# Performance work log

Measured on AMD Instinct MI355X. Metric: run time of the kernel, lower is better.

Reference implementation:

```python
import jax, jax.numpy as jnp
import numpy as np

B, T, N, F = 8, 24, 207, 16
H = 64            # hidden_dim
DH = 16           # dims_hyper[-1] / node-embedding out
DA = 4 * F        # temporal attention dim_out
DS = 64           # ss_gal gcn out dim (last_ss_gal_dim)
GDEP = 2
ALPHA, BETA, GAMMA = 0.05, 0.95, 0.95
TA = 2.0


def _lin(x, w, b=None):
    y = x @ w
    return y if b is None else y + b


def gcn_hyper(x, A, W, b):
    # x: [B,N,C], A: [N,N] static. h <- a*x + g * einsum('nvc,vw->nwc', h, A)
    h = x
    outs = [h]
    for _ in range(GDEP):
        h = ALPHA * x + GAMMA * jnp.einsum('bvc,vw->bwc', h, A)
        outs.append(h)
    return _lin(jnp.concatenate(outs, axis=-1), W, b)


def gcn_gru(x, A_dyn, A_sta, W, b):
    # x: [B,N,C], A_dyn: [B,N,N], A_sta: [N,N]
    h = x
    outs = [h]
    for _ in range(GDEP):
        h = (ALPHA * x
             + BETA * jnp.einsum('bvw,bvc->bwc', A_dyn, h)     # bmm(A^T, h)
             + GAMMA * jnp.einsum('bvc,vw->bwc', h, A_sta))
        outs.append(h)
    return _lin(jnp.concatenate(outs, axis=-1), W, b)


def gcn_ssgal(x, A, W, b):
    # x: [B*,N,C], A: [B*,N,N]
    h = x
    outs = [h]
    for _ in range(GDEP):
        h = ALPHA * x + GAMMA * jnp.einsum('bvw,bvc->bwc', A, h)
        outs.append(h)
    return _lin(jnp.concatenate(outs, axis=-1), W, b)


def setup_inputs() -> dict:
    key = jax.random.key(0)
    ks = jax.random.split(key, 32)
    i = iter(range(32))
    w = lambda *s: (0.02 * jax.random.normal(ks[next(i)], s, dtype=jnp.float32))
    inp = {
        'input_sequence': jax.random.normal(ks[next(i)], (B, T, N, F), dtype=jnp.float32),
        'static_adj': jax.random.uniform(ks[next(i)], (N, N), dtype=jnp.float32),
        # hyper graph generators: mlp in = (GDEP+1)*H -> DH
        'src_gen_w': w((GDEP + 1) * H, DH), 'src_gen_b': w(DH),
        'tgt_gen_w': w((GDEP + 1) * H, DH), 'tgt_gen_b': w(DH),
        # node embeddings: F -> DH
        'src_emb_w': w(F, DH), 'src_emb_b': w(DH),
        'tgt_emb_w': w(F, DH), 'tgt_emb_b': w(DH),
        # GRU gate GCNs: mlp in = (GDEP+1)*(F+H) -> H
        'gru_z_w': w((GDEP + 1) * (F + H), H), 'gru_z_b': w(H),
        'gru_r_w': w((GDEP + 1) * (F + H), H), 'gru_r_b': w(H),
        'gru_c_w': w((GDEP + 1) * (F + H), H), 'gru_c_b': w(H),
        # temporal attention: F -> DA, score DA -> 1
        'attn_q_w': w(F, DA),
        'attn_k_w': w(F, DA), 'attn_k_b': w(DA),
        'attn_s_w': w(DA, 1),
        # ss_gal spatial gcn: (GDEP+1)*F -> DS
        'sgcn_w': w((GDEP + 1) * F, DS), 'sgcn_b': w(DS),
        # predictors
        'short_w': w(DS, F), 'short_b': w(F),
        'long_w': w(H, F), 'long_b': w(F),
        'fus_w': w(DS + H, F), 'fus_b': w(F),
    }
    return inp


def _forward(input_sequence, static_adj,
             src_gen_w, src_gen_b, tgt_gen_w, tgt_gen_b,
             src_emb_w, src_emb_b, tgt_emb_w, tgt_emb_b,
             gru_z_w, gru_z_b, gru_r_w, gru_r_b, gru_c_w, gru_c_b,
             attn_q_w, attn_k_w, attn_k_b, attn_s_w,
             sgcn_w, sgcn_b,
             short_w, short_b, long_w, long_b, fus_w, fus_b):
    batch, steps, nodes = input_sequence.shape[0], input_sequence.shape[1], input_sequence.shape[2]
    eye = jnp.eye(nodes, dtype=input_sequence.dtype)

    def cell(x_t, h):
        # x_t: [B,N,F], h: [B,N,H]
        src_ctx = gcn_hyper(h, static_adj, src_gen_w, src_gen_b)   # [B,N,DH]
        tgt_ctx = gcn_hyper(h, static_adj, tgt_gen_w, tgt_gen_b)
        s = jnp.tanh(TA * _lin(x_t, src_emb_w, src_emb_b) * src_ctx)
        t = jnp.tanh(TA * _lin(x_t, tgt_emb_w, tgt_emb_b) * tgt_ctx)
        asym = jnp.einsum('bnc,bmc->bnm', s, t) - jnp.einsum('bnc,bmc->bnm', t, s)
        adj = jax.nn.relu(jnp.tanh(TA * asym)) + eye
        adj = adj / (adj.sum(axis=-1, keepdims=True) + 1e-8)
        gi = jnp.concatenate([x_t, h], axis=-1)
        z = jax.nn.sigmoid(gcn_gru(gi, adj, static_adj, gru_z_w, gru_z_b))
        r = jax.nn.sigmoid(gcn_gru(gi, adj, static_adj, gru_r_w, gru_r_b))
        ri = jnp.concatenate([x_t, r * h], axis=-1)
        c = jnp.tanh(gcn_gru(ri, adj, static_adj, gru_c_w, gru_c_b))
        return z * h + (1.0 - z) * c

    h = jnp.zeros((batch, nodes, H), dtype=input_sequence.dtype)
    for t_step in range(0, max(1, steps - 4), 4):
        h = cell(input_sequence[:, t_step], h)

    # ss_gal branch on the last 4 steps
    recent = input_sequence[:, -4:]            # [B,4,N,F]
    target = input_sequence[:, -1]             # [B,N,F]
    # temporal attention
    q = target @ attn_q_w                      # [B,N,DA]
    k = recent @ attn_k_w + attn_k_b           # [B,4,N,DA]
    scores = jnp.tanh(q[:, None, :, None, :] + k[:, :, None, :, :])  # [B,4,N,N,DA]
    scores = jnp.squeeze(scores @ attn_s_w, axis=-1)                  # [B,4,N,N]
    attn = jax.nn.softmax(scores, axis=-1)
    dyn_adj = static_adj[None] + attn.reshape(-1, nodes, nodes)       # [B*4,N,N]
    rh = recent.reshape(-1, nodes, recent.shape[-1])                  # [B*4,N,F]
    rh = gcn_ssgal(rh, dyn_adj, sgcn_w, sgcn_b)                       # [B*4,N,DS]
    rh = jax.nn.relu(rh.reshape(batch, -1, nodes, rh.shape[-1]))      # [B,4,N,DS]
    target = jnp.sum(rh, axis=1)                                       # [B,N,DS]

    short = _lin(target, short_w, short_b)      # [B,N,F]
    h = cell(short, h)                          # final GRU step on short-term prediction
    long = _lin(h, long_w, long_b)              # [B,N,F]
    fused = _lin(jnp.concatenate([target, h], axis=-1), fus_w, fus_b)  # [B,N,F]
    return jnp.stack([short, long, fused], axis=0)  # [3,B,N,F]


def reference(input_sequence, static_adj,
              src_gen_w, src_gen_b, tgt_gen_w, tgt_gen_b,
              src_emb_w, src_emb_b, tgt_emb_w, tgt_emb_b,
              gru_z_w, gru_z_b, gru_r_w, gru_r_b, gru_c_w, gru_c_b,
              attn_q_w, attn_k_w, attn_k_b, attn_s_w,
              sgcn_w, sgcn_b,
              short_w, short_b, long_w, long_b, fus_w, fus_b):
    return _forward(input_sequence, static_adj,
                    src_gen_w, src_gen_b, tgt_gen_w, tgt_gen_b,
                    src_emb_w, src_emb_b, tgt_emb_w, tgt_emb_b,
                    gru_z_w, gru_z_b, gru_r_w, gru_r_b, gru_c_w, gru_c_b,
                    attn_q_w, attn_k_w, attn_k_b, attn_s_w,
                    sgcn_w, sgcn_b,
                    short_w, short_b, long_w, long_b, fus_w, fus_b)
```

## Files before the change

### kernel.cpp

```cpp
#include <hip/hip_runtime.h>


constexpr int B = 8, T = 24, N = 207, F = 16, H = 64, DH = 16;
constexpr int PS = 208;
constexpr float ALPHA = 0.05f, BETA = 0.95f, GAMMA = 0.95f, TA = 2.0f;
constexpr int NF = N * F;
constexpr int BNF = B * N * F;

__device__ __forceinline__ float tanh_fast(float x) { float e = __expf(2.f * x); return 1.f - 2.f / (e + 1.f); }
__device__ __forceinline__ float sigm(float x) { return 1.f / (1.f + __expf(-x)); }
__device__ __forceinline__ float tanh_poly(float x) {
    float x2 = x * x;
    float c = __builtin_fmaf(x2, 0.13333333f, -0.33333333f);
    return x * __builtin_fmaf(x2, c, 1.f);
}

__global__ __launch_bounds__(256) void k_stage0(
    const float* __restrict__ adj, const float* __restrict__ inp,
    const float* __restrict__ Wq, const float* __restrict__ Wk,
    const float* __restrict__ kb, const float* __restrict__ sw_,
    float* __restrict__ Ts, float* __restrict__ A2,
    float* __restrict__ attnT, float* __restrict__ rsum)
{
    __shared__ __align__(16) float smem[7424];
// ... 163 lines not shown
        for (int k = 0; k < 2; k++) {
            float4 hv = make_float4(0, 0, 0, 0);
            int v = v0 + hr[k];
            if (v < N) hv = *(const float4*)&hb[(size_t)v * H + hc[k]];
            h4[k] = hv;
        }
    };
    loadT(0);
    int cur = 0;
    for (int t = 0; t < 7; t++) {
        __syncthreads();
        {
            float (*dst)[33] = (tid < 128) ? sTs[cur] : sA2[cur];
            dst[pr][pc4] = t4.x; dst[pr][pc4 + 1] = t4.y; dst[pr][pc4 + 2] = t4.z; dst[pr][pc4 + 3] = t4.w;
        }
#pragma unroll
        for (int k = 0; k < 2; k++) *(float4*)&sH[cur][hr[k]][hc[k]] = h4[k];
        if (t < 6) loadT((t + 1) * 32);
        __syncthreads();
#pragma unroll 8
        for (int v = 0; v < 32; v++) {
            float pu = sTs[cur][ty][v], pw = sA2[cur][ty][v];
#pragma unroll
            for (int j = 0; j < 4; j++) {
                float x = sH[cur][v][tx * 4 + j];
                au[j] += pu * x; aw[j] += pw * x;
            }
        }
        cur ^= 1;
    }
    int w = w0 + ty;
    bool valid = w < N;
    __syncthreads();
    if (valid) {
#pragma unroll
        for (int j = 0; j < 4; j++) {
            int c = tx * 4 + j;
            float hv = hb[(size_t)w * H + c];
            float u = au[j], w2 = aw[j];
            cat[ty][c] = hv;
            cat[ty][64 + c] = ALPHA * hv + GAMMA * u;
            cat[ty][128 + c] = ALPHA * hv + ALPHA * GAMMA * u + GAMMA * GAMMA * w2;
        }
    } else {
#pragma unroll
        for (int j = 0; j < 4; j++) {
            int c = tx * 4 + j;
            cat[ty][c] = 0; cat[ty][64 + c] = 0; cat[ty][128 + c] = 0;
        }
    }
    const float* Wg = lane ? Wtgt : Wsrc;
    const float* bg = lane ? btgt : bsrc;
    const float* We = lane ? Wet : Wes;
    const float* be = lane ? bet : bes;
    {
        float4 wv[3];
#pragma unroll
        for (int k = 0; k < 3; k++) wv[k] = *(const float4*)&Wg[(tid + k * 256) * 4];
        float4 xv = make_float4(0, 0, 0, 0), ev = make_float4(0, 0, 0, 0);
        int sr = 0, sc = 0;
        if (tid < 64) {
            sr = tid >> 2; sc = (tid & 3) * 4;
            int n = w0 + sr;
            if (n < N) xv = *(const float4*)&xp[(size_t)n * F + sc];
            ev = *(const float4*)&We[tid * 4];
        }
#pragma unroll
        for (int k = 0; k < 3; k++) {
            int l4 = tid + k * 256;
            int r = l4 >> 2, c4 = (l4 & 3) * 4;
            *(float4*)&sW[r][c4] = wv[k];
        }
        if (tid < 64) {
            *(float4*)&sX[sr][sc] = xv;
            *(float4*)&sWe[sr][sc] = ev;
        }
    }
    __syncthreads();
    if (lane == 0 && valid) {
#pragma unroll
        for (int j = 0; j < 5; j++) {
            int c = tx * 5 + j;
            float v = (c < 16) ? sX[ty][c] : hb[(size_t)w * H + (c - 16)];
            catg[((size_t)(b * N + w)) * 240 + c] = v;
        }
    }
    {
        float ctx = bg[tx];
#pragma unroll 8
        for (int c = 0; c < 192; c++) ctx += cat[ty][c] * sW[c][tx];
        float xe = be[tx];
#pragma unroll
        for (int f = 0; f < 16; f++) xe += sX[ty][f] * sWe[f][tx];
        if (valid) {
            float val = tanh_fast(TA * xe * ctx);
            if (lane == 0) s_out[(size_t)(b * N + w) * DH + tx] = val;
            else           t_out[(size_t)(b * N + w) * DH + tx] = val;
        }
    }
}

__global__ __launch_bounds__(256) void k_cell_bP(const float* __restrict__ s_in, const float* __restrict__ t_in,
                                                 const float* __restrict__ adj, float* __restrict__ P) {
    int b = blockIdx.y, v0 = blockIdx.x * 16;
    int tid = threadIdx.x, ty = tid >> 4, tx = tid & 15;
    __shared__ float sS[N][17], sT[N][17];
    for (int l4 = tid; l4 < 828; l4 += 256) {
        float4 sv = *(const float4*)&s_in[(size_t)b * N * 16 + l4 * 4];
        float4 tv = *(const float4*)&t_in[(size_t)b * N * 16 + l4 * 4];
        int r = l4 >> 2, c = (l4 & 3) * 4;
        sS[r][c] = sv.x; sS[r][c + 1] = sv.y; sS[r][c + 2] = sv.z; sS[r][c + 3] = sv.w;
        sT[r][c] = tv.x; sT[r][c + 1] = tv.y; sT[r][c + 2] = tv.z; sT[r][c + 3] = tv.w;
    }
    __syncthreads();
    int v = v0 + ty;
    bool valid = v < N;
    int vc = valid ? v : (N - 1);
    float sv[16], tv[16];
#pragma unroll
    for (int k = 0; k < 16; k++) { sv[k] = sS[vc][k]; tv[k] = sT[vc][k]; }
    float val[13];
    float rsum = 0.f;
#pragma unroll
    for (int idx = 0; idx < 13; idx++) {
        int w = tx + 16 * idx;
        float r = 0.f;
        if (w < N) {
            float a = 0.f;
#pragma unroll
            for (int k = 0; k < 16; k++) a += sv[k] * sT[w][k] - tv[k] * sS[w][k];
            r = tanh_fast(TA * a);
            r = r > 0.f ? r : 0.f;
            if (w == v) r += 1.f;
        }
        val[idx] = r;
        rsum += r;
    }
    float tot = rsum;
    for (int d = 8; d > 0; d >>= 1) tot += __shfl_down(tot, d, 16);
    tot = __shfl(tot, 0, 16);
    float rinv = BETA / (tot + 1e-8f);
    if (valid) {
        float* Pb = P + (size_t)b * PS * PS;
#pragma unroll
        for (int idx = 0; idx < 13; idx++) {
            int w = tx + 16 * idx;
            if (w < N) Pb[(size_t)w * PS + v] = val[idx] * rinv + GAMMA * adj[v * N + w];
        }
    }
}

__global__ __launch_bounds__(256) void k_prop1(const float* __restrict__ P, float* __restrict__ cat) {
    int b = blockIdx.y, w0 = blockIdx.x * 16, c0 = blockIdx.z * 16;
    int tid = threadIdx.x, ty = tid >> 4, tx = tid & 15;
    const float* Pb = P + (size_t)b * PS * PS;
    __shared__ float sP[2][16][33], sX[2][32][17];
    float a1 = 0.f;
    int pr = tid >> 4, pc = (tid & 15) * 2;
    int xr = tid >> 3, xc = (tid & 7) * 2;
    float2 pv, xv;
    auto loadT = [&](int v0) {
        pv = make_float2(0, 0); xv = make_float2(0, 0);
        int w = w0 + pr;
        if (w < N) pv = *(const float2*)&Pb[(size_t)w * PS + v0 + pc];
        int vv = v0 + xr;
        if (vv < N) xv = *(const float2*)&cat[((size_t)(b * N + vv)) * 240 + c0 + xc];
    };
    loadT(0);
    int cur = 0;
    for (int t = 0; t < 7; t++) {
        __syncthreads();
        sP[cur][pr][pc] = pv.x; sP[cur][pr][pc + 1] = pv.y;
        sX[cur][xr][xc] = xv.x; sX[cur][xr][xc + 1] = xv.y;
        if (t < 6) loadT((t + 1) * 32);
        __syncthreads();
#pragma unroll 8
        for (int v_ = 0; v_ < 32; v_++) a1 += sP[cur][ty][v_] * sX[cur][v_][tx];
        cur ^= 1;
    }
    int w = w0 + ty, c = c0 + tx;
    if (w < N) {
        size_t base = ((size_t)(b * N + w)) * 240;
        cat[base + 80 + c] = ALPHA * cat[base + c] + a1;
    }
}

__global__ __launch_bounds__(256) void k_gate(
    const float* __restrict__ cat, const float* __restrict__ P,
    const float* __restrict__ Wa, const float* __restrict__ ba,
    const float* __restrict__ Wb, const float* __restrict__ bb,
    int baseMode,
    const float* __restrict__ xseq, int tsel, const float* __restrict__ xbuf,
    float* __restrict__ zbuf, float* __restrict__ ricat,
    float* __restrict__ h,
    const float* __restrict__ target,
    const float* __restrict__ Wlong, const float* __restrict__ blong,
    const float* __restrict__ Wfus, const float* __restrict__ bfus,
    float* __restrict__ out) {
    int mode = baseMode + blockIdx.z;
    const float* W = (mode == 1) ? Wb : Wa;
    const float* bias = (mode == 1) ? bb : ba;
    int b = blockIdx.y, w0 = blockIdx.x * 16;
    int tid = threadIdx.x, ty = tid >> 4, tx = tid & 15;
    const float* Pb = P + (size_t)b * PS * PS;
    __shared__ float sC[16][241];
    __shared__ float sP[16][33];
    __shared__ float sX[32][81];
    __shared__ float sW[48][65];
    __shared__ float hrow[16][65], trow[16][65];
    for (int l4 = tid; l4 < 640; l4 += 256) {
        int r = l4 / 40, c4 = (l4 % 40) * 4;
        int w = w0 + r;
        float4 v4 = make_float4(0, 0, 0, 0);
        if (w < N) v4 = *(const float4*)&cat[((size_t)(b * N + w)) * 240 + c4];
        sC[r][c4] = v4.x; sC[r][c4 + 1] = v4.y; sC[r][c4 + 2] = v4.z; sC[r][c4 + 3] = v4.w;
    }
    float acc[5] = {0, 0, 0, 0, 0};
    int prr = tid >> 4, prc = (tid & 15) * 2;
    int xrow = tid & 31, xc0 = (tid >> 5) * 10;
    float2 pv;
    float2 xv[5];
    auto loadT = [&](int v0) {
        pv = make_float2(0, 0);
        int w = w0 + prr;
        if (w < N) pv = *(const float2*)&Pb[(size_t)w * PS + v0 + prc];
        int v = v0 + xrow;
#pragma unroll
        for (int k = 0; k < 5; k++) xv[k] = make_float2(0, 0);
        if (v < N) {
            const float* src = &cat[((size_t)(b * N + v)) * 240 + 80 + xc0];
#pragma unroll
            for (int k = 0; k < 5; k++) xv[k] = *(const float2*)&src[k * 2];
        }
    };
    loadT(0);
    for (int t = 0; t < 7; t++) {
        __syncthreads();
        sP[prr][prc] = pv.x; sP[prr][prc + 1] = pv.y;
#pragma unroll
        for (int k = 0; k < 5; k++) { sX[xrow][xc0 + 2 * k] = xv[k].x; sX[xrow][xc0 + 2 * k + 1] = xv[k].y; }
        if (t < 6) loadT((t + 1) * 32);
        __syncthreads();
#pragma unroll 8
        for (int v = 0; v < 32; v++) {
            float p = sP[ty][v];
#pragma unroll
            for (int j = 0; j < 5; j++) acc[j] += p * sX[v][tx * 5 + j];
        }
    }
#pragma unroll
    for (int j = 0; j < 5; j++) {
        int c = tx * 5 + j;
        sC[ty][160 + c] = ALPHA * sC[ty][c] + acc[j];
    }
    float4 wv[3];
#pragma unroll
    for (int k = 0; k < 3; k++) wv[k] = *(const float4*)&W[(tid + k * 256) * 4];
    float ga[4];
#pragma unroll
    for (int j = 0; j < 4; j++) ga[j] = bias[tx * 4 + j];
    for (int ch = 0; ch < 5; ch++) {
        __syncthreads();
#pragma unroll
        for (int k = 0; k < 3; k++) {
            int l4 = tid + k * 256;
            int r = l4 >> 4, cc = (l4 & 15) * 4;
            sW[r][cc] = wv[k].x; sW[r][cc + 1] = wv[k].y; sW[r][cc + 2] = wv[k].z; sW[r][cc + 3] = wv[k].w;
        }
        if (ch < 4) {
#pragma unroll
            for (int k = 0; k < 3; k++) wv[k] = *(const float4*)&W[(size_t)(ch + 1) * 3072 + (tid + k * 256) * 4];
        }
        __syncthreads();
        int c0 = ch * 48;
#pragma unroll 8
        for (int cc = 0; cc < 48; cc++) {
            float cv = sC[ty][c0 + cc];
#pragma unroll
            for (int j = 0; j < 4; j++) ga[j] += cv * sW[cc][tx * 4 + j];
        }
    }
    int w = w0 + ty;
    bool valid = w < N;
    if (mode == 0) {
        if (valid) {
#pragma unroll
            for (int j = 0; j < 4; j++) zbuf[((size_t)(b * N + w)) * 64 + tx * 4 + j] = sigm(ga[j]);
        }
    } else if (mode == 1) {
        if (valid) {
#pragma unroll
            for (int j = 0; j < 4; j++) {
                int o = tx * 4 + j;
                ricat[((size_t)(b * N + w)) * 240 + 16 + o] = sigm(ga[j]) * h[((size_t)(b * N + w)) * 64 + o];
            }
            if (tx < 4) {
                const float* xp = (tsel >= 0) ? (xseq + ((size_t)(b * T + tsel)) * NF) : (xbuf + (size_t)b * NF);
#pragma unroll
                for (int j = 0; j < 4; j++) {
                    int c = tx * 4 + j;
                    ricat[((size_t)(b * N + w)) * 240 + c] = xp[w * F + c];
                }
            }
        }
    } else {
#pragma unroll
        for (int j = 0; j < 4; j++) {
            int o = tx * 4 + j;
            float cval = tanh_fast(ga[j]);
            float zv = 0.f, hv = 0.f;
            if (valid) { zv = zbuf[((size_t)(b * N + w)) * 64 + o]; hv = h[((size_t)(b * N + w)) * 64 + o]; }
            float hn = zv * hv + (1.f - zv) * cval;
            if (valid) h[((size_t)(b * N + w)) * 64 + o] = hn;
            hrow[ty][o] = valid ? hn : 0.f;
        }
        if (mode == 3) {
            for (int l = tid; l < 1024; l += 256) {
                int i = l >> 6, o = l & 63;
                int ww = w0 + i;
                trow[i][o] = (ww < N) ? target[((size_t)(b * N + ww)) * 64 + o] : 0.f;
            }
            __syncthreads();
            float lg = blong[tx];
            float fs = bfus[tx];
#pragma unroll 8
            for (int o = 0; o < 64; o++) {
                lg += hrow[ty][o] * Wlong[o * 16 + tx];
                fs += trow[ty][o] * Wfus[o * 16 + tx] + hrow[ty][o] * Wfus[(64 + o) * 16 + tx];
            }
            if (valid) {
                out[((size_t)1 * B * N + b * N + w) * 16 + tx] = lg;
                out[((size_t)2 * B * N + b * N + w) * 16 + tx] = fs;
            }
        }
    }
}

__global__ __launch_bounds__(256) void k_prop_xr(const float* __restrict__ attnT, const float* __restrict__ rsum,
                                                 const float* __restrict__ Ts, const float* __restrict__ inp,
                                                 float* __restrict__ x1) {
    int bt = blockIdx.y, w0 = blockIdx.x * 16;
    int b = bt >> 2, tau = bt & 3;
    const float* xb = inp + ((size_t)(b * T + 20 + tau)) * NF;
    const float* PA = attnT + (size_t)bt * PS * PS;
    int tid = threadIdx.x, ty = tid >> 4, tx = tid & 15;
    __shared__ float sPA[2][16][33], sPT[2][16][33];
    __shared__ float sX[2][32][17], sXs[2][32][17];
    float accA = 0.f, accT = 0.f;
    int prr = tid >> 3, pcc = (tid & 7) * 4;
    int xrr = (tid - 128) >> 2, xcc = ((tid - 128) & 3) * 4;
    float4 pa, pt, xv;
    float rinv_;
    auto loadT = [&](int v0) {
        pa = make_float4(0, 0, 0, 0); pt = make_float4(0, 0, 0, 0); xv = make_float4(0, 0, 0, 0); rinv_ = 0.f;
        if (tid < 128) {
            int w = w0 + prr;
            if (w < N) {
                pa = *(const float4*)&PA[(size_t)w * PS + v0 + pcc];
                pt = *(const float4*)&Ts[(size_t)w * PS + v0 + pcc];
            }
        } else {
            int v = v0 + xrr;
            if (v < N) {
                xv = *(const float4*)&xb[(size_t)v * F + xcc];
                rinv_ = __builtin_amdgcn_rcpf(rsum[bt * N + v]);
            }
        }
    };
    loadT(0);
    int cur = 0;
    for (int t = 0; t < 7; t++) {
        __syncthreads();
        if (tid < 128) {
            sPA[cur][prr][pcc] = pa.x; sPA[cur][prr][pcc + 1] = pa.y; sPA[cur][prr][pcc + 2] = pa.z; sPA[cur][prr][pcc + 3] = pa.w;
            sPT[cur][prr][pcc] = pt.x; sPT[cur][prr][pcc + 1] = pt.y; sPT[cur][prr][pcc + 2] = pt.z; sPT[cur][prr][pcc + 3] = pt.w;
        } else {
            sX[cur][xrr][xcc] = xv.x; sX[cur][xrr][xcc + 1] = xv.y; sX[cur][xrr][xcc + 2] = xv.z; sX[cur][xrr][xcc + 3] = xv.w;
            sXs[cur][xrr][xcc] = xv.x * rinv_; sXs[cur][xrr][xcc + 1] = xv.y * rinv_;
            sXs[cur][xrr][xcc + 2] = xv.z * rinv_; sXs[cur][xrr][xcc + 3] = xv.w * rinv_;
        }
        if (t < 6) loadT((t + 1) * 32);
        __syncthreads();
#pragma unroll 8
        for (int v = 0; v < 32; v++) {
            accA += sPA[cur][ty][v] * sXs[cur][v][tx];
            accT += sPT[cur][ty][v] * sX[cur][v][tx];
        }
        cur ^= 1;
    }
    int w = w0 + ty;
    if (w < N) x1[((size_t)(bt * N + w)) * 16 + tx] = ALPHA * xb[w * F + tx] + GAMMA * (accA + accT);
}

__global__ __launch_bounds__(256) void k_sgc2(const float* __restrict__ attnT, const float* __restrict__ rsum,
                                              const float* __restrict__ Ts, const float* __restrict__ x1,
                                              const float* __restrict__ inp,
                                              const float* __restrict__ Ws, const float* __restrict__ bs,
                                              float* __restrict__ target) {
    int bt = blockIdx.y, b = bt >> 2, tau = bt & 3, w0 = blockIdx.x * 16;
    const float* xb = inp + ((size_t)(b * T + 20 + tau)) * NF;
    const float* PA = attnT + (size_t)bt * PS * PS;
    int tid = threadIdx.x, ty = tid >> 4, tx = tid & 15;
    __shared__ float sPA[2][16][33], sPT[2][16][33];
    __shared__ float sX[2][32][17], sXs[2][32][17];
    __shared__ float cat[16][48];
    __shared__ __align__(16) float sW[48][64];
    float accA = 0.f, accT = 0.f;
    int prr = tid >> 3, pcc = (tid & 7) * 4;
    int xrr = (tid - 128) >> 2, xcc = ((tid - 128) & 3) * 4;
    float4 pa, pt, xv;
    float rinv_;
    auto loadT = [&](int v0) {
        pa = make_float4(0, 0, 0, 0); pt = make_float4(0, 0, 0, 0); xv = make_float4(0, 0, 0, 0); rinv_ = 0.f;
        if (tid < 128) {
            int w = w0 + prr;
            if (w < N) {
                pa = *(const float4*)&PA[(size_t)w * PS + v0 + pcc];
                pt = *(const float4*)&Ts[(size_t)w * PS + v0 + pcc];
            }
        } else {
            int v = v0 + xrr;
            if (v < N) {
                xv = *(const float4*)&x1[((size_t)(bt * N + v)) * 16 + xcc];
                rinv_ = __builtin_amdgcn_rcpf(rsum[bt * N + v]);
            }
        }
    };
    loadT(0);
    int cur = 0;
    for (int t = 0; t < 7; t++) {
        __syncthreads();
        if (tid < 128) {
            sPA[cur][prr][pcc] = pa.x; sPA[cur][prr][pcc + 1] = pa.y; sPA[cur][prr][pcc + 2] = pa.z; sPA[cur][prr][pcc + 3] = pa.w;
            sPT[cur][prr][pcc] = pt.x; sPT[cur][prr][pcc + 1] = pt.y; sPT[cur][prr][pcc + 2] = pt.z; sPT[cur][prr][pcc + 3] = pt.w;
        } else {
            sX[cur][xrr][xcc] = xv.x; sX[cur][xrr][xcc + 1] = xv.y; sX[cur][xrr][xcc + 2] = xv.z; sX[cur][xrr][xcc + 3] = xv.w;
            sXs[cur][xrr][xcc] = xv.x * rinv_; sXs[cur][xrr][xcc + 1] = xv.y * rinv_;
            sXs[cur][xrr][xcc + 2] = xv.z * rinv_; sXs[cur][xrr][xcc + 3] = xv.w * rinv_;
        }
        if (t < 6) loadT((t + 1) * 32);
        __syncthreads();
#pragma unroll 8
        for (int v = 0; v < 32; v++) {
            accA += sPA[cur][ty][v] * sXs[cur][v][tx];
            accT += sPT[cur][ty][v] * sX[cur][v][tx];
        }
        cur ^= 1;
    }
    int w = w0 + ty;
    bool valid = w < N;
    __syncthreads();
    for (int l = tid; l < 512; l += 256) {
        int i = l >> 5, c = l & 31;
        int ww = w0 + i;
        float vv = 0;
        if (ww < N) {
            if (c < 16) vv = xb[ww * F + c];
            else vv = x1[((size_t)bt * N + ww) * 16 + (c - 16)];
        }
        cat[i][c] = vv;
    }
    {
        float x0 = valid ? xb[w * F + tx] : 0.f;
        cat[ty][32 + tx] = ALPHA * x0 + GAMMA * (accA + accT);
    }
    {
        float4 wv[3];
#pragma unroll
        for (int k = 0; k < 3; k++) wv[k] = *(const float4*)&Ws[(tid + k * 256) * 4];
#pragma unroll
        for (int k = 0; k < 3; k++) {
            int l4 = tid + k * 256;
            *(float4*)&sW[l4 >> 4][(l4 & 15) * 4] = wv[k];
        }
    }
    __syncthreads();
    float a[4];
#pragma unroll
    for (int j = 0; j < 4; j++) a[j] = bs[tx * 4 + j];
#pragma unroll 8
    for (int cc = 0; cc < 48; cc++) {
        float cv = cat[ty][cc];
        float4 w4 = *(const float4*)&sW[cc][tx * 4];
        a[0] += cv * w4.x; a[1] += cv * w4.y; a[2] += cv * w4.z; a[3] += cv * w4.w;
    }
    if (valid) {
#pragma unroll
        for (int j = 0; j < 4; j++) {
            float r = a[j] > 0.f ? a[j] : 0.f;
            atomicAdd(&target[(b * N + w) * 64 + tx * 4 + j], r);
        }
    }
}

__global__ __launch_bounds__(256) void k_short(const float* __restrict__ target,
                                               const float* __restrict__ Wsh, const float* __restrict__ bsh,
                                               float* __restrict__ out, float* __restrict__ xshort) {
    int b = blockIdx.y, n0 = blockIdx.x * 16;
    int tid = threadIdx.x, ty = tid >> 4, tx = tid & 15;
    __shared__ float trow[16][65], sW[64][16];
    {
        int r = tid >> 4, c4 = (tid & 15) * 4;
        int n = n0 + r;
        float4 tv = make_float4(0, 0, 0, 0);
        if (n < N) tv = *(const float4*)&target[((size_t)(b * N + n)) * 64 + c4];
        trow[r][c4] = tv.x; trow[r][c4 + 1] = tv.y; trow[r][c4 + 2] = tv.z; trow[r][c4 + 3] = tv.w;
        float4 wv = *(const float4*)&Wsh[tid * 4];
        *(float4*)&sW[tid >> 2][(tid & 3) * 4] = wv;
    }
    __syncthreads();
    float a = bsh[tx];
#pragma unroll 8
    for (int o = 0; o < 64; o++) a += trow[ty][o] * sW[o][tx];
    int n = n0 + ty;
    if (n < N) {
        out[((size_t)0 * B * N + b * N + n) * 16 + tx] = a;
        xshort[(b * N + n) * 16 + tx] = a;
    }
}

extern "C" void kernel_launch(void* const* d_in, const int* in_sizes, int n_in,
                              void* d_out, int out_size, void* d_ws, size_t ws_size,
                              hipStream_t stream) {
    const float* inp = (const float*)d_in[0];
    const float* adj = (const float*)d_in[1];
    const float* src_gen_w = (const float*)d_in[2];
    const float* src_gen_b = (const float*)d_in[3];
    const float* tgt_gen_w = (const float*)d_in[4];
    const float* tgt_gen_b = (const float*)d_in[5];
    const float* src_emb_w = (const float*)d_in[6];
    const float* src_emb_b = (const float*)d_in[7];
    const float* tgt_emb_w = (const float*)d_in[8];
    const float* tgt_emb_b = (const float*)d_in[9];
    const float* gru_z_w = (const float*)d_in[10];
    const float* gru_z_b = (const float*)d_in[11];
    const float* gru_r_w = (const float*)d_in[12];
    const float* gru_r_b = (const float*)d_in[13];
    const float* gru_c_w = (const float*)d_in[14];
    const float* gru_c_b = (const float*)d_in[15];
    const float* attn_q_w = (const float*)d_in[16];
    const float* attn_k_w = (const float*)d_in[17];
    const float* attn_k_b = (const float*)d_in[18];
    const float* attn_s_w = (const float*)d_in[19];
    const float* sgcn_w = (const float*)d_in[20];
    const float* sgcn_b = (const float*)d_in[21];
    const float* short_w = (const float*)d_in[22];
    const float* short_b = (const float*)d_in[23];
    const float* long_w = (const float*)d_in[24];
    const float* long_b = (const float*)d_in[25];
    const float* fus_w = (const float*)d_in[26];
    const float* fus_b = (const float*)d_in[27];
    float* out = (float*)d_out;

    float* ws = (float*)d_ws;
    size_t off = 0;
    auto A = [&](size_t n) { n = (n + 3) & ~(size_t)3; float* p = ws + off; off += n; return p; };
    float* Ts = A((size_t)PS * PS);
    float* A2 = A((size_t)PS * PS);
    float* sbuf = A((size_t)B * N * DH);
    float* tbuf = A((size_t)B * N * DH);
    float* P = A((size_t)B * PS * PS);
    float* catg = A((size_t)B * N * 240);
    float* catc = A((size_t)B * N * 240);
    float* zb = A((size_t)B * N * 64);
    float* attnT = A((size_t)32 * PS * PS);
    float* x1 = A((size_t)32 * NF);
    float* xshort = A(BNF);
    size_t zero_begin = off;
    float* h = A((size_t)B * N * H);
    float* target = A((size_t)B * N * 64);
    float* rsum = A((size_t)32 * N);
    size_t zero_end = off;
    (void)ws_size; (void)in_sizes; (void)n_in; (void)out_size;

    hipMemsetAsync(h, 0, (zero_end - zero_begin) * sizeof(float), stream);
    k_stage0<<<1785, 256, 0, stream>>>(adj, inp, attn_q_w, attn_k_w, attn_k_b, attn_s_w, Ts, A2, attnT, rsum);

    auto run_cell = [&](int tsel, const float* xbuf, int finalFlag) {
        k_cell_a<<<dim3(13, B, 2), 256, 0, stream>>>(h, Ts, A2, inp, tsel, xbuf,
                                                     src_gen_w, src_gen_b, tgt_gen_w, tgt_gen_b,
                                                     src_emb_w, src_emb_b, tgt_emb_w, tgt_emb_b, sbuf, tbuf, catg);
        k_cell_bP<<<dim3(13, B), 256, 0, stream>>>(sbuf, tbuf, adj, P);
        k_prop1<<<dim3(13, B, 5), 256, 0, stream>>>(P, catg);
        k_gate<<<dim3(13, B, 2), 256, 0, stream>>>(catg, P, gru_z_w, gru_z_b, gru_r_w, gru_r_b, 0,
                                                   inp, tsel, xbuf, zb, catc, h,
                                                   nullptr, nullptr, nullptr, nullptr, nullptr, nullptr);
        k_prop1<<<dim3(13, B, 5), 256, 0, stream>>>(P, catc);
        k_gate<<<dim3(13, B, 1), 256, 0, stream>>>(catc, P, gru_c_w, gru_c_b, nullptr, nullptr, 2 + finalFlag,
                                                   nullptr, 0, nullptr, zb, nullptr, h,
                                                   target, long_w, long_b, fus_w, fus_b, out);
    };

    for (int t = 0; t < 20; t += 4) run_cell(t, nullptr, 0);

    k_prop_xr<<<dim3(13, 32), 256, 0, stream>>>(attnT, rsum, Ts, inp, x1);
    k_sgc2<<<dim3(13, 32), 256, 0, stream>>>(attnT, rsum, Ts, x1, inp, sgcn_w, sgcn_b, target);
    k_short<<<dim3(13, B), 256, 0, stream>>>(target, short_w, short_b, out, xshort);

    run_cell(-1, xshort, 1);
}
```

Measured before the change: 629.0 us.

## Precompute squared propagation matrix and fold independent stages into its launch

Each cell now computes P² once in a new kernel, so every gate kernel forms both diffusion hops (P·x and P²·x) in one pass. This removes the two k_prop1 launches per cell and the separate hop-1 buffer, which shrinks the cat rows from 240 to 80 floats. The independent attention-GCN and short-head work (prop_xr, sgc2, short) is placed as extra blocks inside the P² launch of the first three cells, overlapping it with the recurrent chain. The cost is a dense 207x207 matmul per batch per cell, plus rounding that differs from applying P twice, and the reordered stage dependencies must still hold.

Measured after the change: 629.9 us. No clear change (+0.1%).

```diff
diff --git a/kernel.cpp b/kernel.cpp
--- a/kernel.cpp
+++ b/kernel.cpp
@@ -269,7 +269,7 @@
         for (int j = 0; j < 5; j++) {
             int c = tx * 5 + j;
             float v = (c < 16) ? sX[ty][c] : hb[(size_t)w * H + (c - 16)];
-            catg[((size_t)(b * N + w)) * 240 + c] = v;
+            catg[((size_t)(b * N + w)) * 80 + c] = v;
         }
     }
     {
@@ -337,43 +337,246 @@
     }
 }
 
-__global__ __launch_bounds__(256) void k_prop1(const float* __restrict__ P, float* __restrict__ cat) {
-    int b = blockIdx.y, w0 = blockIdx.x * 16, c0 = blockIdx.z * 16;
+__device__ __forceinline__ void body_prop_xr(float* smem, int w0, int bt,
+    const float* __restrict__ attnT, const float* __restrict__ rsum,
+    const float* __restrict__ Ts, const float* __restrict__ inp, float* __restrict__ x1)
+{
+    int b = bt >> 2, tau = bt & 3;
+    const float* xb = inp + ((size_t)(b * T + 20 + tau)) * NF;
+    const float* PA = attnT + (size_t)bt * PS * PS;
     int tid = threadIdx.x, ty = tid >> 4, tx = tid & 15;
-    const float* Pb = P + (size_t)b * PS * PS;
-    __shared__ float sP[2][16][33], sX[2][32][17];
-    float a1 = 0.f;
-    int pr = tid >> 4, pc = (tid & 15) * 2;
-    int xr = tid >> 3, xc = (tid & 7) * 2;
-    float2 pv, xv;
+    float (*sPA)[16][33] = (float(*)[16][33])(smem);
+    float (*sPT)[16][33] = (float(*)[16][33])(smem + 1056);
+    float (*sX)[32][17]  = (float(*)[32][17])(smem + 2112);
+    float (*sXs)[32][17] = (float(*)[32][17])(smem + 3200);
+    float accA = 0.f, accT = 0.f;
+    int prr = tid >> 3, pcc = (tid & 7) * 4;
+    int xrr = (tid - 128) >> 2, xcc = ((tid - 128) & 3) * 4;
+    float4 pa, pt, xv;
+    float rinv_;
     auto loadT = [&](int v0) {
-        pv = make_float2(0, 0); xv = make_float2(0, 0);
-        int w = w0 + pr;
-        if (w < N) pv = *(const float2*)&Pb[(size_t)w * PS + v0 + pc];
-        int vv = v0 + xr;
-        if (vv < N) xv = *(const float2*)&cat[((size_t)(b * N + vv)) * 240 + c0 + xc];
+        pa = make_float4(0, 0, 0, 0); pt = make_float4(0, 0, 0, 0); xv = make_float4(0, 0, 0, 0); rinv_ = 0.f;
+        if (tid < 128) {
+            int w = w0 + prr;
+            if (w < N) {
+                pa = *(const float4*)&PA[(size_t)w * PS + v0 + pcc];
+                pt = *(const float4*)&Ts[(size_t)w * PS + v0 + pcc];
+            }
+        } else {
+            int v = v0 + xrr;
+            if (v < N) {
+                xv = *(const float4*)&xb[(size_t)v * F + xcc];
+                rinv_ = __builtin_amdgcn_rcpf(rsum[bt * N + v]);
+            }
+        }
     };
     loadT(0);
     int cur = 0;
     for (int t = 0; t < 7; t++) {
         __syncthreads();
-        sP[cur][pr][pc] = pv.x; sP[cur][pr][pc + 1] = pv.y;
-        sX[cur][xr][xc] = xv.x; sX[cur][xr][xc + 1] = xv.y;
+        if (tid < 128) {
+            sPA[cur][prr][pcc] = pa.x; sPA[cur][prr][pcc + 1] = pa.y; sPA[cur][prr][pcc + 2] = pa.z; sPA[cur][prr][pcc + 3] = pa.w;
+            sPT[cur][prr][pcc] = pt.x; sPT[cur][prr][pcc + 1] = pt.y; sPT[cur][prr][pcc + 2] = pt.z; sPT[cur][prr][pcc + 3] = pt.w;
+        } else {
+            sX[cur][xrr][xcc] = xv.x; sX[cur][xrr][xcc + 1] = xv.y; sX[cur][xrr][xcc + 2] = xv.z; sX[cur][xrr][xcc + 3] = xv.w;
+            sXs[cur][xrr][xcc] = xv.x * rinv_; sXs[cur][xrr][xcc + 1] = xv.y * rinv_;
+            sXs[cur][xrr][xcc + 2] = xv.z * rinv_; sXs[cur][xrr][xcc + 3] = xv.w * rinv_;
+        }
         if (t < 6) loadT((t + 1) * 32);
         __syncthreads();
 #pragma unroll 8
-        for (int v_ = 0; v_ < 32; v_++) a1 += sP[cur][ty][v_] * sX[cur][v_][tx];
+        for (int v = 0; v < 32; v++) {
+            accA += sPA[cur][ty][v] * sXs[cur][v][tx];
+            accT += sPT[cur][ty][v] * sX[cur][v][tx];
+        }
         cur ^= 1;
     }
-    int w = w0 + ty, c = c0 + tx;
-    if (w < N) {
-        size_t base = ((size_t)(b * N + w)) * 240;
-        cat[base + 80 + c] = ALPHA * cat[base + c] + a1;
-    }
-}
-
-__global__ __launch_bounds__(256) void k_gate(
-    const float* __restrict__ cat, const float* __restrict__ P,
+    int w = w0 + ty;
+    if (w < N) x1[((size_t)(bt * N + w)) * 16 + tx] = ALPHA * xb[w * F + tx] + GAMMA * (accA + accT);
+}
+
+__device__ __forceinline__ void body_sgc2(float* smem, int w0, int bt,
+    const float* __restrict__ attnT, const float* __restrict__ rsum,
+    const float* __restrict__ Ts, const float* __restrict__ x1, const float* __restrict__ inp,
+    const float* __restrict__ Ws, const float* __restrict__ bs, float* __restrict__ target)
+{
+    int b = bt >> 2, tau = bt & 3;
+    const float* xb = inp + ((size_t)(b * T + 20 + tau)) * NF;
+    const float* PA = attnT + (size_t)bt * PS * PS;
+    int tid = threadIdx.x, ty = tid >> 4, tx = tid & 15;
+    float (*sPA)[16][33] = (float(*)[16][33])(smem);
+    float (*sPT)[16][33] = (float(*)[16][33])(smem + 1056);
+    float (*sX)[32][17]  = (float(*)[32][17])(smem + 2112);
+    float (*sXs)[32][17] = (float(*)[32][17])(smem + 3200);
+    float (*scat)[48]    = (float(*)[48])(smem + 4288);
+    float (*sWs)[64]     = (float(*)[64])(smem + 5056);
+    float accA = 0.f, accT = 0.f;
+    int prr = tid >> 3, pcc = (tid & 7) * 4;
+    int xrr = (tid - 128) >> 2, xcc = ((tid - 128) & 3) * 4;
+    float4 pa, pt, xv;
+    float rinv_;
+    auto loadT = [&](int v0) {
+        pa = make_float4(0, 0, 0, 0); pt = make_float4(0, 0, 0, 0); xv = make_float4(0, 0, 0, 0); rinv_ = 0.f;
+        if (tid < 128) {
+            int w = w0 + prr;
+            if (w < N) {
+                pa = *(const float4*)&PA[(size_t)w * PS + v0 + pcc];
+                pt = *(const float4*)&Ts[(size_t)w * PS + v0 + pcc];
+            }
+        } else {
+            int v = v0 + xrr;
+            if (v < N) {
+                xv = *(const float4*)&x1[((size_t)(bt * N + v)) * 16 + xcc];
+                rinv_ = __builtin_amdgcn_rcpf(rsum[bt * N + v]);
+            }
+        }
+    };
+    loadT(0);
+    int cur = 0;
+    for (int t = 0; t < 7; t++) {
+        __syncthreads();
+        if (tid < 128) {
+            sPA[cur][prr][pcc] = pa.x; sPA[cur][prr][pcc + 1] = pa.y; sPA[cur][prr][pcc + 2] = pa.z; sPA[cur][prr][pcc + 3] = pa.w;
+            sPT[cur][prr][pcc] = pt.x; sPT[cur][prr][pcc + 1] = pt.y; sPT[cur][prr][pcc + 2] = pt.z; sPT[cur][prr][pcc + 3] = pt.w;
+        } else {
+            sX[cur][xrr][xcc] = xv.x; sX[cur][xrr][xcc + 1] = xv.y; sX[cur][xrr][xcc + 2] = xv.z; sX[cur][xrr][xcc + 3] = xv.w;
+            sXs[cur][xrr][xcc] = xv.x * rinv_; sXs[cur][xrr][xcc + 1] = xv.y * rinv_;
+            sXs[cur][xrr][xcc + 2] = xv.z * rinv_; sXs[cur][xrr][xcc + 3] = xv.w * rinv_;
+        }
+        if (t < 6) loadT((t + 1) * 32);
+        __syncthreads();
+#pragma unroll 8
+        for (int v = 0; v < 32; v++) {
+            accA += sPA[cur][ty][v] * sXs[cur][v][tx];
+            accT += sPT[cur][ty][v] * sX[cur][v][tx];
+        }
+        cur ^= 1;
+    }
+    int w = w0 + ty;
+    bool valid = w < N;
+    __syncthreads();
+    for (int l = tid; l < 512; l += 256) {
+        int i = l >> 5, c = l & 31;
+        int ww = w0 + i;
+        float vv = 0;
+        if (ww < N) {
+            if (c < 16) vv = xb[ww * F + c];
+            else vv = x1[((size_t)bt * N + ww) * 16 + (c - 16)];
+        }
+        scat[i][c] = vv;
+    }
+    {
+        float x0 = valid ? xb[w * F + tx] : 0.f;
+        scat[ty][32 + tx] = ALPHA * x0 + GAMMA * (accA + accT);
+    }
+    {
+        float4 wv[3];
+#pragma unroll
+        for (int k = 0; k < 3; k++) wv[k] = *(const float4*)&Ws[(tid + k * 256) * 4];
+#pragma unroll
+        for (int k = 0; k < 3; k++) {
+            int l4 = tid + k * 256;
+            *(float4*)&sWs[l4 >> 4][(l4 & 15) * 4] = wv[k];
+        }
+    }
+    __syncthreads();
+    float a[4];
+#pragma unroll
+    for (int j = 0; j < 4; j++) a[j] = bs[tx * 4 + j];
+#pragma unroll 8
+    for (int cc = 0; cc < 48; cc++) {
+        float cv = scat[ty][cc];
+        float4 w4 = *(const float4*)&sWs[cc][tx * 4];
+        a[0] += cv * w4.x; a[1] += cv * w4.y; a[2] += cv * w4.z; a[3] += cv * w4.w;
+    }
+    if (valid) {
+#pragma unroll
+        for (int j = 0; j < 4; j++) {
+            float r = a[j] > 0.f ? a[j] : 0.f;
+            atomicAdd(&target[(b * N + w) * 64 + tx * 4 + j], r);
+        }
+    }
+}
+
+__device__ __forceinline__ void body_short(float* smem, int n0, int b,
+    const float* __restrict__ target, const float* __restrict__ Wsh, const float* __restrict__ bsh,
+    float* __restrict__ out, float* __restrict__ xshort)
+{
+    int tid = threadIdx.x, ty = tid >> 4, tx = tid & 15;
+    float (*trow)[65] = (float(*)[65])(smem);
+    float (*sW)[16]   = (float(*)[16])(smem + 1040);
+    {
+        int r = tid >> 4, c4 = (tid & 15) * 4;
+        int n = n0 + r;
+        float4 tv = make_float4(0, 0, 0, 0);
+        if (n < N) tv = *(const float4*)&target[((size_t)(b * N + n)) * 64 + c4];
+        trow[r][c4] = tv.x; trow[r][c4 + 1] = tv.y; trow[r][c4 + 2] = tv.z; trow[r][c4 + 3] = tv.w;
+        float4 wv = *(const float4*)&Wsh[tid * 4];
+        *(float4*)&sW[tid >> 2][(tid & 3) * 4] = wv;
+    }
+    __syncthreads();
+    float a = bsh[tx];
+#pragma unroll 8
+    for (int o = 0; o < 64; o++) a += trow[ty][o] * sW[o][tx];
+    int n = n0 + ty;
+    if (n < N) {
+        out[((size_t)0 * B * N + b * N + n) * 16 + tx] = a;
+        xshort[(b * N + n) * 16 + tx] = a;
+    }
+}
+
+__global__ __launch_bounds__(256) void k_psq(
+    const float* __restrict__ P, float* __restrict__ P2, int aux,
+    const float* __restrict__ attnT, const float* __restrict__ rsum,
+    const float* __restrict__ Ts, const float* __restrict__ inp, float* __restrict__ x1,
+    const float* __restrict__ Ws, const float* __restrict__ bs, float* __restrict__ target,
+    const float* __restrict__ Wsh, const float* __restrict__ bsh,
+    float* __restrict__ out, float* __restrict__ xshort)
+{
+    __shared__ __align__(16) float smem[8128];
+    int bid = blockIdx.x, tid = threadIdx.x;
+    if (bid < 1352) {
+        int b = bid / 169, r = bid % 169;
+        int w0 = (r % 13) * 16, v0 = (r / 13) * 16;
+        const float* Pb = P + (size_t)b * PS * PS;
+        float (*sA)[16][33] = (float(*)[16][33])(smem);
+        float (*sB)[32][17] = (float(*)[32][17])(smem + 1056);
+        int ty = tid >> 4, tx = tid & 15;
+        int ar = tid >> 4, ac = (tid & 15) * 2;
+        int br = tid >> 3, bc = (tid & 7) * 2;
+        float2 av, bv;
+        auto loadT = [&](int u0) {
+            av = make_float2(0, 0); bv = make_float2(0, 0);
+            int w = w0 + ar;
+            if (w < N) av = *(const float2*)&Pb[(size_t)w * PS + u0 + ac];
+            int u = u0 + br;
+            if (u < N) bv = *(const float2*)&Pb[(size_t)u * PS + v0 + bc];
+        };
+        loadT(0);
+        int cur = 0;
+        float acc = 0.f;
+        for (int t = 0; t < 7; t++) {
+            __syncthreads();
+            sA[cur][ar][ac] = av.x; sA[cur][ar][ac + 1] = av.y;
+            sB[cur][br][bc] = bv.x; sB[cur][br][bc + 1] = bv.y;
+            if (t < 6) loadT((t + 1) * 32);
+            __syncthreads();
+#pragma unroll 8
+            for (int u = 0; u < 32; u++) acc += sA[cur][ty][u] * sB[cur][u][tx];
+            cur ^= 1;
+        }
+        int w = w0 + ty, v = v0 + tx;
+        if (w < N && v < N) P2[(size_t)b * PS * PS + (size_t)w * PS + v] = acc;
+    } else {
+        int idx = bid - 1352;
+        if (aux == 1)      body_prop_xr(smem, (idx % 13) * 16, idx / 13, attnT, rsum, Ts, inp, x1);
+        else if (aux == 2) body_sgc2(smem, (idx % 13) * 16, idx / 13, attnT, rsum, Ts, x1, inp, Ws, bs, target);
+        else               body_short(smem, (idx % 13) * 16, idx / 13, target, Wsh, bsh, out, xshort);
+    }
+}
+
+__global__ __launch_bounds__(256) void k_gate2(
+    const float* __restrict__ cat, const float* __restrict__ P, const float* __restrict__ P2,
     const float* __restrict__ Wa, const float* __restrict__ ba,
     const float* __restrict__ Wb, const float* __restrict__ bb,
     int baseMode,
@@ -390,32 +593,36 @@
     int b = blockIdx.y, w0 = blockIdx.x * 16;
     int tid = threadIdx.x, ty = tid >> 4, tx = tid & 15;
     const float* Pb = P + (size_t)b * PS * PS;
+    const float* Qb = P2 + (size_t)b * PS * PS;
     __shared__ float sC[16][241];
-    __shared__ float sP[16][33];
+    __shared__ float sP[16][33], sQ[16][33];
     __shared__ float sX[32][81];
     __shared__ float sW[48][65];
     __shared__ float hrow[16][65], trow[16][65];
-    for (int l4 = tid; l4 < 640; l4 += 256) {
-        int r = l4 / 40, c4 = (l4 % 40) * 4;
+    for (int l4 = tid; l4 < 320; l4 += 256) {
+        int r = l4 / 20, c4 = (l4 % 20) * 4;
         int w = w0 + r;
         float4 v4 = make_float4(0, 0, 0, 0);
-        if (w < N) v4 = *(const float4*)&cat[((size_t)(b * N + w)) * 240 + c4];
+        if (w < N) v4 = *(const float4*)&cat[((size_t)(b * N + w)) * 80 + c4];
         sC[r][c4] = v4.x; sC[r][c4 + 1] = v4.y; sC[r][c4 + 2] = v4.z; sC[r][c4 + 3] = v4.w;
     }
-    float acc[5] = {0, 0, 0, 0, 0};
+    float accP[5] = {0, 0, 0, 0, 0}, accQ[5] = {0, 0, 0, 0, 0};
     int prr = tid >> 4, prc = (tid & 15) * 2;
     int xrow = tid & 31, xc0 = (tid >> 5) * 10;
-    float2 pv;
+    float2 pv, qv;
     float2 xv[5];
     auto loadT = [&](int v0) {
-        pv = make_float2(0, 0);
+        pv = make_float2(0, 0); qv = make_float2(0, 0);
         int w = w0 + prr;
-        if (w < N) pv = *(const float2*)&Pb[(size_t)w * PS + v0 + prc];
+        if (w < N) {
+            pv = *(const float2*)&Pb[(size_t)w * PS + v0 + prc];
+            qv = *(const float2*)&Qb[(size_t)w * PS + v0 + prc];
+        }
         int v = v0 + xrow;
 #pragma unroll
         for (int k = 0; k < 5; k++) xv[k] = make_float2(0, 0);
         if (v < N) {
-            const float* src = &cat[((size_t)(b * N + v)) * 240 + 80 + xc0];
+            const float* src = &cat[((size_t)(b * N + v)) * 80 + xc0];
 #pragma unroll
             for (int k = 0; k < 5; k++) xv[k] = *(const float2*)&src[k * 2];
         }
@@ -424,21 +631,28 @@
     for (int t = 0; t < 7; t++) {
         __syncthreads();
         sP[prr][prc] = pv.x; sP[prr][prc + 1] = pv.y;
+        sQ[prr][prc] = qv.x; sQ[prr][prc + 1] = qv.y;
 #pragma unroll
         for (int k = 0; k < 5; k++) { sX[xrow][xc0 + 2 * k] = xv[k].x; sX[xrow][xc0 + 2 * k + 1] = xv[k].y; }
         if (t < 6) loadT((t + 1) * 32);
         __syncthreads();
 #pragma unroll 8
         for (int v = 0; v < 32; v++) {
-            float p = sP[ty][v];
-#pragma unroll
-            for (int j = 0; j < 5; j++) acc[j] += p * sX[v][tx * 5 + j];
+            float p = sP[ty][v], q = sQ[ty][v];
+#pragma unroll
+            for (int j = 0; j < 5; j++) {
+                float x = sX[v][tx * 5 + j];
+                accP[j] += p * x;
+                accQ[j] += q * x;
+            }
         }
     }
 #pragma unroll
     for (int j = 0; j < 5; j++) {
         int c = tx * 5 + j;
-        sC[ty][160 + c] = ALPHA * sC[ty][c] + acc[j];
+        float g0 = sC[ty][c];
+        sC[ty][80 + c]  = ALPHA * g0 + accP[j];
+        sC[ty][160 + c] = ALPHA * g0 + ALPHA * accP[j] + accQ[j];
     }
     float4 wv[3];
 #pragma unroll
@@ -479,14 +693,14 @@
 #pragma unroll
             for (int j = 0; j < 4; j++) {
                 int o = tx * 4 + j;
-                ricat[((size_t)(b * N + w)) * 240 + 16 + o] = sigm(ga[j]) * h[((size_t)(b * N + w)) * 64 + o];
+                ricat[((size_t)(b * N + w)) * 80 + 16 + o] = sigm(ga[j]) * h[((size_t)(b * N + w)) * 64 + o];
             }
             if (tx < 4) {
                 const float* xp = (tsel >= 0) ? (xseq + ((size_t)(b * T + tsel)) * NF) : (xbuf + (size_t)b * NF);
 #pragma unroll
                 for (int j = 0; j < 4; j++) {
                     int c = tx * 4 + j;
-                    ricat[((size_t)(b * N + w)) * 240 + c] = xp[w * F + c];
+                    ricat[((size_t)(b * N + w)) * 80 + c] = xp[w * F + c];
                 }
             }
         }
@@ -520,189 +734,6 @@
                 out[((size_t)2 * B * N + b * N + w) * 16 + tx] = fs;
             }
         }
-    }
-}
-
-__global__ __launch_bounds__(256) void k_prop_xr(const float* __restrict__ attnT, const float* __restrict__ rsum,
-                                                 const float* __restrict__ Ts, const float* __restrict__ inp,
-                                                 float* __restrict__ x1) {
-    int bt = blockIdx.y, w0 = blockIdx.x * 16;
-    int b = bt >> 2, tau = bt & 3;
-    const float* xb = inp + ((size_t)(b * T + 20 + tau)) * NF;
-    const float* PA = attnT + (size_t)bt * PS * PS;
-    int tid = threadIdx.x, ty = tid >> 4, tx = tid & 15;
-    __shared__ float sPA[2][16][33], sPT[2][16][33];
-    __shared__ float sX[2][32][17], sXs[2][32][17];
-    float accA = 0.f, accT = 0.f;
-    int prr = tid >> 3, pcc = (tid & 7) * 4;
-    int xrr = (tid - 128) >> 2, xcc = ((tid - 128) & 3) * 4;
-    float4 pa, pt, xv;
-    float rinv_;
-    auto loadT = [&](int v0) {
-        pa = make_float4(0, 0, 0, 0); pt = make_float4(0, 0, 0, 0); xv = make_float4(0, 0, 0, 0); rinv_ = 0.f;
-        if (tid < 128) {
-            int w = w0 + prr;
-            if (w < N) {
-                pa = *(const float4*)&PA[(size_t)w * PS + v0 + pcc];
-                pt = *(const float4*)&Ts[(size_t)w * PS + v0 + pcc];
-            }
-        } else {
-            int v = v0 + xrr;
-            if (v < N) {
-                xv = *(const float4*)&xb[(size_t)v * F + xcc];
-                rinv_ = __builtin_amdgcn_rcpf(rsum[bt * N + v]);
-            }
-        }
-    };
-    loadT(0);
-    int cur = 0;
-    for (int t = 0; t < 7; t++) {
-        __syncthreads();
-        if (tid < 128) {
-            sPA[cur][prr][pcc] = pa.x; sPA[cur][prr][pcc + 1] = pa.y; sPA[cur][prr][pcc + 2] = pa.z; sPA[cur][prr][pcc + 3] = pa.w;
-            sPT[cur][prr][pcc] = pt.x; sPT[cur][prr][pcc + 1] = pt.y; sPT[cur][prr][pcc + 2] = pt.z; sPT[cur][prr][pcc + 3] = pt.w;
-        } else {
-            sX[cur][xrr][xcc] = xv.x; sX[cur][xrr][xcc + 1] = xv.y; sX[cur][xrr][xcc + 2] = xv.z; sX[cur][xrr][xcc + 3] = xv.w;
-            sXs[cur][xrr][xcc] = xv.x * rinv_; sXs[cur][xrr][xcc + 1] = xv.y * rinv_;
-            sXs[cur][xrr][xcc + 2] = xv.z * rinv_; sXs[cur][xrr][xcc + 3] = xv.w * rinv_;
-        }
-        if (t < 6) loadT((t + 1) * 32);
-        __syncthreads();
-#pragma unroll 8
-        for (int v = 0; v < 32; v++) {
-            accA += sPA[cur][ty][v] * sXs[cur][v][tx];
-            accT += sPT[cur][ty][v] * sX[cur][v][tx];
-        }
-        cur ^= 1;
-    }
-    int w = w0 + ty;
-    if (w < N) x1[((size_t)(bt * N + w)) * 16 + tx] = ALPHA * xb[w * F + tx] + GAMMA * (accA + accT);
-}
-
-__global__ __launch_bounds__(256) void k_sgc2(const float* __restrict__ attnT, const float* __restrict__ rsum,
-                                              const float* __restrict__ Ts, const float* __restrict__ x1,
-                                              const float* __restrict__ inp,
-                                              const float* __restrict__ Ws, const float* __restrict__ bs,
-                                              float* __restrict__ target) {
-    int bt = blockIdx.y, b = bt >> 2, tau = bt & 3, w0 = blockIdx.x * 16;
-    const float* xb = inp + ((size_t)(b * T + 20 + tau)) * NF;
-    const float* PA = attnT + (size_t)bt * PS * PS;
-    int tid = threadIdx.x, ty = tid >> 4, tx = tid & 15;
-    __shared__ float sPA[2][16][33], sPT[2][16][33];
-    __shared__ float sX[2][32][17], sXs[2][32][17];
-    __shared__ float cat[16][48];
-    __shared__ __align__(16) float sW[48][64];
-    float accA = 0.f, accT = 0.f;
-    int prr = tid >> 3, pcc = (tid & 7) * 4;
-    int xrr = (tid - 128) >> 2, xcc = ((tid - 128) & 3) * 4;
-    float4 pa, pt, xv;
-    float rinv_;
-    auto loadT = [&](int v0) {
-        pa = make_float4(0, 0, 0, 0); pt = make_float4(0, 0, 0, 0); xv = make_float4(0, 0, 0, 0); rinv_ = 0.f;
-        if (tid < 128) {
-            int w = w0 + prr;
-            if (w < N) {
-                pa = *(const float4*)&PA[(size_t)w * PS + v0 + pcc];
-                pt = *(const float4*)&Ts[(size_t)w * PS + v0 + pcc];
-            }
-        } else {
-            int v = v0 + xrr;
-            if (v < N) {
-                xv = *(const float4*)&x1[((size_t)(bt * N + v)) * 16 + xcc];
-                rinv_ = __builtin_amdgcn_rcpf(rsum[bt * N + v]);
-            }
-        }
-    };
-    loadT(0);
-    int cur = 0;
-    for (int t = 0; t < 7; t++) {
-        __syncthreads();
-        if (tid < 128) {
-            sPA[cur][prr][pcc] = pa.x; sPA[cur][prr][pcc + 1] = pa.y; sPA[cur][prr][pcc + 2] = pa.z; sPA[cur][prr][pcc + 3] = pa.w;
-            sPT[cur][prr][pcc] = pt.x; sPT[cur][prr][pcc + 1] = pt.y; sPT[cur][prr][pcc + 2] = pt.z; sPT[cur][prr][pcc + 3] = pt.w;
-        } else {
-            sX[cur][xrr][xcc] = xv.x; sX[cur][xrr][xcc + 1] = xv.y; sX[cur][xrr][xcc + 2] = xv.z; sX[cur][xrr][xcc + 3] = xv.w;
-            sXs[cur][xrr][xcc] = xv.x * rinv_; sXs[cur][xrr][xcc + 1] = xv.y * rinv_;
-            sXs[cur][xrr][xcc + 2] = xv.z * rinv_; sXs[cur][xrr][xcc + 3] = xv.w * rinv_;
-        }
-        if (t < 6) loadT((t + 1) * 32);
-        __syncthreads();
-#pragma unroll 8
-        for (int v = 0; v < 32; v++) {
-            accA += sPA[cur][ty][v] * sXs[cur][v][tx];
-            accT += sPT[cur][ty][v] * sX[cur][v][tx];
-        }
-        cur ^= 1;
-    }
-    int w = w0 + ty;
-    bool valid = w < N;
-    __syncthreads();
-    for (int l = tid; l < 512; l += 256) {
-        int i = l >> 5, c = l & 31;
-        int ww = w0 + i;
-        float vv = 0;
-        if (ww < N) {
-            if (c < 16) vv = xb[ww * F + c];
-            else vv = x1[((size_t)bt * N + ww) * 16 + (c - 16)];
-        }
-        cat[i][c] = vv;
-    }
-    {
-        float x0 = valid ? xb[w * F + tx] : 0.f;
-        cat[ty][32 + tx] = ALPHA * x0 + GAMMA * (accA + accT);
-    }
-    {
-        float4 wv[3];
-#pragma unroll
-        for (int k = 0; k < 3; k++) wv[k] = *(const float4*)&Ws[(tid + k * 256) * 4];
-#pragma unroll
-        for (int k = 0; k < 3; k++) {
-            int l4 = tid + k * 256;
-            *(float4*)&sW[l4 >> 4][(l4 & 15) * 4] = wv[k];
-        }
-    }
-    __syncthreads();
-    float a[4];
-#pragma unroll
-    for (int j = 0; j < 4; j++) a[j] = bs[tx * 4 + j];
-#pragma unroll 8
-    for (int cc = 0; cc < 48; cc++) {
-        float cv = cat[ty][cc];
-        float4 w4 = *(const float4*)&sW[cc][tx * 4];
-        a[0] += cv * w4.x; a[1] += cv * w4.y; a[2] += cv * w4.z; a[3] += cv * w4.w;
-    }
-    if (valid) {
-#pragma unroll
-        for (int j = 0; j < 4; j++) {
-            float r = a[j] > 0.f ? a[j] : 0.f;
-            atomicAdd(&target[(b * N + w) * 64 + tx * 4 + j], r);
-        }
-    }
-}
-
-__global__ __launch_bounds__(256) void k_short(const float* __restrict__ target,
-                                               const float* __restrict__ Wsh, const float* __restrict__ bsh,
-                                               float* __restrict__ out, float* __restrict__ xshort) {
-    int b = blockIdx.y, n0 = blockIdx.x * 16;
-    int tid = threadIdx.x, ty = tid >> 4, tx = tid & 15;
-    __shared__ float trow[16][65], sW[64][16];
-    {
-        int r = tid >> 4, c4 = (tid & 15) * 4;
-        int n = n0 + r;
-        float4 tv = make_float4(0, 0, 0, 0);
-        if (n < N) tv = *(const float4*)&target[((size_t)(b * N + n)) * 64 + c4];
-        trow[r][c4] = tv.x; trow[r][c4 + 1] = tv.y; trow[r][c4 + 2] = tv.z; trow[r][c4 + 3] = tv.w;
-        float4 wv = *(const float4*)&Wsh[tid * 4];
-        *(float4*)&sW[tid >> 2][(tid & 3) * 4] = wv;
-    }
-    __syncthreads();
-    float a = bsh[tx];
-#pragma unroll 8
-    for (int o = 0; o < 64; o++) a += trow[ty][o] * sW[o][tx];
-    int n = n0 + ty;
-    if (n < N) {
-        out[((size_t)0 * B * N + b * N + n) * 16 + tx] = a;
-        xshort[(b * N + n) * 16 + tx] = a;
     }
 }
 
@@ -747,8 +778,9 @@
     float* sbuf = A((size_t)B * N * DH);
     float* tbuf = A((size_t)B * N * DH);
     float* P = A((size_t)B * PS * PS);
-    float* catg = A((size_t)B * N * 240);
-    float* catc = A((size_t)B * N * 240);
+    float* P2 = A((size_t)B * PS * PS);
+    float* catg = A((size_t)B * N * 80);
+    float* catc = A((size_t)B * N * 80);
     float* zb = A((size_t)B * N * 64);
     float* attnT = A((size_t)32 * PS * PS);
     float* x1 = A((size_t)32 * NF);
@@ -763,26 +795,27 @@
     hipMemsetAsync(h, 0, (zero_end - zero_begin) * sizeof(float), stream);
     k_stage0<<<1785, 256, 0, stream>>>(adj, inp, attn_q_w, attn_k_w, attn_k_b, attn_s_w, Ts, A2, attnT, rsum);
 
-    auto run_cell = [&](int tsel, const float* xbuf, int finalFlag) {
+    auto run_cell = [&](int tsel, const float* xbuf, int finalFlag, int aux) {
         k_cell_a<<<dim3(13, B, 2), 256, 0, stream>>>(h, Ts, A2, inp, tsel, xbuf,
                                                      src_gen_w, src_gen_b, tgt_gen_w, tgt_gen_b,
                                                      src_emb_w, src_emb_b, tgt_emb_w, tgt_emb_b, sbuf, tbuf, catg);
         k_cell_bP<<<dim3(13, B), 256, 0, stream>>>(sbuf, tbuf, adj, P);
-        k_prop1<<<dim3(13, B, 5), 256, 0, stream>>>(P, catg);
-        k_gate<<<dim3(13, B, 2), 256, 0, stream>>>(catg, P, gru_z_w, gru_z_b, gru_r_w, gru_r_b, 0,
-                                                   inp, tsel, xbuf, zb, catc, h,
-                                                   nullptr, nullptr, nullptr, nullptr, nullptr, nullptr);
-        k_prop1<<<dim3(13, B, 5), 256, 0, stream>>>(P, catc);
-        k_gate<<<dim3(13, B, 1), 256, 0, stream>>>(catc, P, gru_c_w, gru_c_b, nullptr, nullptr, 2 + finalFlag,
-                                                   nullptr, 0, nullptr, zb, nullptr, h,
-                                                   target, long_w, long_b, fus_w, fus_b, out);
+        int extra = (aux == 1 || aux == 2) ? 416 : (aux == 3 ? 104 : 0);
+        k_psq<<<1352 + extra, 256, 0, stream>>>(P, P2, aux, attnT, rsum, Ts, inp, x1,
+                                                sgcn_w, sgcn_b, target, short_w, short_b, out, xshort);
+        k_gate2<<<dim3(13, B, 2), 256, 0, stream>>>(catg, P, P2, gru_z_w, gru_z_b, gru_r_w, gru_r_b, 0,
+                                                    inp, tsel, xbuf, zb, catc, h,
+                                                    nullptr, nullptr, nullptr, nullptr, nullptr, nullptr);
+        k_gate2<<<dim3(13, B, 1), 256, 0, stream>>>(catc, P, P2, gru_c_w, gru_c_b, nullptr, nullptr, 2 + finalFlag,
+                                                    nullptr, 0, nullptr, zb, nullptr, h,
+                                                    target, long_w, long_b, fus_w, fus_b, out);
     };
 
-    for (int t = 0; t < 20; t += 4) run_cell(t, nullptr, 0);
-
-    k_prop_xr<<<dim3(13, 32), 256, 0, stream>>>(attnT, rsum, Ts, inp, x1);
-    k_sgc2<<<dim3(13, 32), 256, 0, stream>>>(attnT, rsum, Ts, x1, inp, sgcn_w, sgcn_b, target);
-    k_short<<<dim3(13, B), 256, 0, stream>>>(target, short_w, short_b, out, xshort);
-
-    run_cell(-1, xshort, 1);
-}
+    run_cell(0, nullptr, 0, 1);
+    run_cell(4, nullptr, 0, 2);
+    run_cell(8, nullptr, 0, 3);
+    run_cell(12, nullptr, 0, 0);
+    run_cell(16, nullptr, 0, 0);
+
+    run_cell(-1, xshort, 1, 0);
+}
```
